# Kernel tuning notes

Hardware: AMD Instinct MI355X
Metric: run time of the kernel (lower is better)

## Reference

```python
import jax, jax.numpy as jnp
import numpy as np
from jax import lax

DIM = 1024
EXPAND = 2
D_STATE = 16
D_CONV = 4
DT_RANK = 64  # ceil(DIM/16)
DIM_INNER = DIM * EXPAND
B_SZ, SEQ = 2, 1024


def setup_inputs() -> dict:
    key = jax.random.key(0)
    ks = jax.random.split(key, 8)
    s = lambda fan_in: 1.0 / np.sqrt(fan_in)
    x = jax.random.normal(ks[0], (B_SZ, SEQ, DIM), dtype=jnp.float32)
    W_in = jax.random.normal(ks[1], (DIM, 2 * DIM_INNER), dtype=jnp.float32) * s(DIM)
    conv_w = jax.random.normal(ks[2], (DIM_INNER, D_CONV), dtype=jnp.float32) * s(D_CONV)
    conv_b = jax.random.normal(ks[3], (DIM_INNER,), dtype=jnp.float32) * s(D_CONV)
    W_x = jax.random.normal(ks[4], (DIM_INNER, DT_RANK + 2 * D_STATE), dtype=jnp.float32) * s(DIM_INNER)
    W_dt = jax.random.normal(ks[5], (DT_RANK, DIM_INNER), dtype=jnp.float32) * s(DT_RANK)
    b_dt = jax.random.normal(ks[6], (DIM_INNER,), dtype=jnp.float32) * s(DT_RANK)
    # A_log = log(repeat(arange(1, d_state+1), 'n -> d n'))
    A_log = jnp.broadcast_to(jnp.log(jnp.arange(1, D_STATE + 1, dtype=jnp.float32)), (DIM_INNER, D_STATE))
    D = jnp.ones((DIM_INNER,), dtype=jnp.float32)
    W_out = jax.random.normal(ks[7], (DIM_INNER, DIM), dtype=jnp.float32) * s(DIM_INNER)
    return {"x": x, "W_in": W_in, "conv_w": conv_w, "conv_b": conv_b,
            "W_x": W_x, "W_dt": W_dt, "b_dt": b_dt, "A_log": A_log, "D": D, "W_out": W_out}


def _mamba_forward(x, W_in, conv_w, conv_b, W_x, W_dt, b_dt, A_log, D, W_out):
    b, l, d = x.shape
    di = W_out.shape[0]  # dim_inner
    n = A_log.shape[1]   # d_state
    dt_rank = W_dt.shape[0]

    # in_proj (no bias) and split into ssm branch / gate residual
    x_and_res = x @ W_in                      # [b, l, 2*di]
    u, res = jnp.split(x_and_res, 2, axis=-1)  # each [b, l, di]

    # causal depthwise conv1d along sequence (torch pads both sides then slices [:l])
    pad = conv_w.shape[1] - 1
    up = jnp.pad(u, ((0, 0), (pad, 0), (0, 0)))
    kernel = conv_w.T[:, None, :]  # [W=d_conv, I=1, O=di]
    u = lax.conv_general_dilated(up, kernel, window_strides=(1,), padding='VALID',
                                 dimension_numbers=('NWC', 'WIO', 'NWC'),
                                 feature_group_count=di) + conv_b
    u = jax.nn.silu(u)  # [b, l, di]

    # input-dependent SSM params
    x_dbl = u @ W_x  # [b, l, dt_rank + 2n]
    delta_r, Bm, Cm = jnp.split(x_dbl, [dt_rank, dt_rank + n], axis=-1)
    delta = jax.nn.softplus(delta_r @ W_dt + b_dt)  # [b, l, di]
    A = -jnp.exp(A_log)  # [di, n]

    deltaA = jnp.exp(jnp.einsum('bld,dn->bldn', delta, A))        # [b, l, di, n]
    deltaB_u = jnp.einsum('bld,bln,bld->bldn', delta, Bm, u)       # [b, l, di, n]

    def step(h, inp):
        dA_t, dBu_t, c_t = inp            # [b,di,n], [b,di,n], [b,n]
        h = dA_t * h + dBu_t
        y_t = jnp.einsum('bdn,bn->bd', h, c_t)
        return h, y_t

    h0 = jnp.zeros((b, di, n), dtype=u.dtype)
    xs = (jnp.moveaxis(deltaA, 1, 0), jnp.moveaxis(deltaB_u, 1, 0), jnp.moveaxis(Cm, 1, 0))
    _, ys = lax.scan(step, h0, xs)        # ys: [l, b, di]
    y = jnp.moveaxis(ys, 0, 1)            # [b, l, di]
    y = y + u * D                          # skip term

    y = y * jax.nn.silu(res)               # gate
    return y @ W_out                       # [b, l, dim]


def reference(x, W_in, conv_w, conv_b, W_x, W_dt, b_dt, A_log, D, W_out):
    return _mamba_forward(x, W_in, conv_w, conv_b, W_x, W_dt, b_dt, A_log, D, W_out)
```

## Files before the change

kernel.cpp:

```cpp
#include <hip/hip_runtime.h>
#include <hip/hip_bf16.h>
#include <math.h>


__device__ __forceinline__ float silu_f(float x) {
    return x / (1.f + __expf(-x));
}
__device__ __forceinline__ unsigned short f2bf(float f) {
    __hip_bfloat16 h = __float2bfloat16(f);
    return *(unsigned short*)&h;
}
__device__ __forceinline__ float bf2f(unsigned short u) {
    return __uint_as_float((unsigned)u << 16);
}

typedef __attribute__((ext_vector_type(8))) short short8v;
typedef __attribute__((ext_vector_type(4))) float f32x4;

__device__ __forceinline__ void gload16(const void* g, void* lds) {
    __builtin_amdgcn_global_load_lds(
        (const __attribute__((address_space(1))) unsigned int*)g,
        (__attribute__((address_space(3))) unsigned int*)lds, 16, 0, 0);
}

template<int MODE>
__device__ __forceinline__ void gemm_core(
    const unsigned short* __restrict__ A,
    const unsigned short* __restrict__ BT,
    float* __restrict__ C, unsigned short* __restrict__ Cb,
    int M, int N, int K, int kbeg, int klen,
    int bx, int by, unsigned short* As, unsigned short* Bs)
{
    const int tid  = threadIdx.x;
    const int wid  = tid >> 6;
    const int lane = tid & 63;
    const int wr = wid >> 1, wc = wid & 1;
    const int row0 = by * 128, col0 = bx * 128;

    f32x4 acc[4][4] = {};

    const int srow = lane >> 2;
    const int scol = (lane & 3) * 8;

    for (int k0 = kbeg; k0 < kbeg + klen; k0 += 32) {
        #pragma unroll
        for (int c = 0; c < 2; ++c) {
            int chunk = wid * 2 + c;
            gload16(A  + (size_t)(row0 + chunk * 16 + srow) * K + k0 + scol,
                    (void*)(As + chunk * 512));
            gload16(BT + (size_t)(col0 + chunk * 16 + srow) * K + k0 + scol,
                    (void*)(Bs + chunk * 512));
        }
        __syncthreads();
        short8v a[4], b[4];
        #pragma unroll
        for (int i = 0; i < 4; ++i)
            a[i] = *(const short8v*)&As[(wr * 64 + i * 16 + (lane & 15)) * 32 + (lane >> 4) * 8];
        #pragma unroll
        for (int j = 0; j < 4; ++j)
            b[j] = *(const short8v*)&Bs[(wc * 64 + j * 16 + (lane & 15)) * 32 + (lane >> 4) * 8];
        #pragma unroll
        for (int i = 0; i < 4; ++i)
            #pragma unroll
            for (int j = 0; j < 4; ++j)
                acc[i][j] = __builtin_amdgcn_mfma_f32_16x16x32_bf16(a[i], b[j], acc[i][j], 0, 0, 0);
        __syncthreads();
    }

    #pragma unroll
    for (int i = 0; i < 4; ++i) {
        int rbase = row0 + wr * 64 + i * 16 + (lane >> 4) * 4;
        #pragma unroll
        for (int j = 0; j < 4; ++j) {
            int cc = col0 + wc * 64 + j * 16 + (lane & 15);
            #pragma unroll
            for (int r = 0; r < 4; ++r) {
                float v = acc[i][j][r];
                if (MODE == 0) {
                    C[(size_t)(rbase + r) * N + cc] = v;
                } else {
                    unsigned short m = f2bf(v);
                    unsigned other = (unsigned)__shfl_xor((int)m, 1, 64) & 0xffffu;
                    if (!(lane & 1))
                        *(unsigned*)(Cb + (size_t)(rbase + r) * N + cc) =
                            (unsigned)m | (other << 16);
                }
            }
        }
    }
}

__global__ __launch_bounds__(256) void gemm7_swz(
    const unsigned short* __restrict__ A,
    const unsigned short* __restrict__ BT,
    unsigned short* __restrict__ Pb)
{
    __shared__ unsigned short As[128 * 32];
    __shared__ unsigned short Bs[128 * 32];
    const int bid = blockIdx.x;
    const int xcd = bid & 7, idx = bid >> 3;
    const int kz = xcd >> 1;
    const int by = (xcd & 1) * 8 + (idx >> 3);
    const int bx = idx & 7;
    gemm_core<4>(A, BT, nullptr, Pb + (size_t)kz * 2048 * 1024,
                 2048, 1024, 2048, kz * 512, 512, bx, by, As, Bs);
}

template<int MODE>
__global__ __launch_bounds__(256) void gemm64_bf16(
    const unsigned short* __restrict__ A,
    const unsigned short* __restrict__ BT,
    unsigned short* __restrict__ Cb,
    const float* __restrict__ bias,
    int M, int N, int K, int klen)
{
    __shared__ unsigned short As[64 * 32];
    __shared__ unsigned short Bs[64 * 32];
    const int tid  = threadIdx.x;
    const int wid  = tid >> 6;
    const int lane = tid & 63;
    const int wr = wid >> 1, wc = wid & 1;
    const int row0 = blockIdx.y * 64, col0 = blockIdx.x * 64;
    const int kbeg = blockIdx.z * klen;
    if (MODE == 5) Cb += (size_t)blockIdx.z * M * N;

    f32x4 acc[2][2] = {};
    const int srow = lane >> 2;
    const int scol = (lane & 3) * 8;

    for (int k0 = kbeg; k0 < kbeg + klen; k0 += 32) {
        gload16(A  + (size_t)(row0 + wid * 16 + srow) * K + k0 + scol,
                (void*)(As + wid * 512));
        gload16(BT + (size_t)(col0 + wid * 16 + srow) * K + k0 + scol,
                (void*)(Bs + wid * 512));
        __syncthreads();
        short8v a[2], b[2];
        #pragma unroll
        for (int i = 0; i < 2; ++i)
            a[i] = *(const short8v*)&As[(wr * 32 + i * 16 + (lane & 15)) * 32 + (lane >> 4) * 8];
        #pragma unroll
        for (int j = 0; j < 2; ++j)
            b[j] = *(const short8v*)&Bs[(wc * 32 + j * 16 + (lane & 15)) * 32 + (lane >> 4) * 8];
        #pragma unroll
        for (int i = 0; i < 2; ++i)
            #pragma unroll
            for (int j = 0; j < 2; ++j)
                acc[i][j] = __builtin_amdgcn_mfma_f32_16x16x32_bf16(a[i], b[j], acc[i][j], 0, 0, 0);
        __syncthreads();
    }

    #pragma unroll
    for (int i = 0; i < 2; ++i) {
        int rbase = row0 + wr * 32 + i * 16 + (lane >> 4) * 4;
        #pragma unroll
        for (int j = 0; j < 2; ++j) {
            int cc = col0 + wc * 32 + j * 16 + (lane & 15);
            float bi = (MODE == 3) ? bias[cc] : 0.f;
            #pragma unroll
            for (int r = 0; r < 4; ++r) {
                float v = acc[i][j][r];
                if (MODE == 3) {
                    v += bi;
                    v = (v > 20.f) ? v : __logf(1.f + __expf(v));
                }
                unsigned short m = f2bf(v);
                unsigned other = (unsigned)__shfl_xor((int)m, 1, 64) & 0xffffu;
                if (!(lane & 1))
                    *(unsigned*)(Cb + (size_t)(rbase + r) * N + cc) =
                        (unsigned)m | (other << 16);
            }
        }
    }
}

__device__ __forceinline__ void trans64(
    const float* __restrict__ W, unsigned short* __restrict__ WT,
    int K, int N, int bk, int bn, int tid, float (*t)[65])
{
    const int tx = tid & 63, ty = tid >> 6;
    #pragma unroll
    for (int s = 0; s < 16; ++s)
        t[ty + 4 * s][tx] = W[(size_t)(bk + ty + 4 * s) * N + bn + tx];
    __syncthreads();
    const int c = tid & 31, rg = tid >> 5;
    #pragma unroll
    for (int s = 0; s < 8; ++s) {
        int r = rg + 8 * s;
        unsigned lo = f2bf(t[2 * c][r]);
        unsigned hi = f2bf(t[2 * c + 1][r]);
        *(unsigned*)(WT + (size_t)(bn + r) * K + bk + 2 * c) = lo | (hi << 16);
    }
}

__global__ __launch_bounds__(256) void gemm1_fused(
    const unsigned short* __restrict__ xb,
    const unsigned short* __restrict__ W_inT,
    unsigned short* __restrict__ xrb,
    const float* __restrict__ W_out,
    const float* __restrict__ Wx,
    const float* __restrict__ Wdt,
    unsigned short* __restrict__ W_outT,
    unsigned short* __restrict__ W_xTp,
    unsigned short* __restrict__ W_dtTp)
{
    __shared__ char smem[64 * 65 * 4];
    const int bid = blockIdx.x;
    const int tid = threadIdx.x;
    if (bid < 512) {
        unsigned short* As = (unsigned short*)smem;
        unsigned short* Bs = As + 128 * 32;
        const int xcd = bid & 7, idx = bid >> 3;
        const int bx = (xcd & 3) * 8 + (idx & 7);
        const int by = (xcd >> 2) * 8 + (idx >> 3);
        gemm_core<4>(xb, W_inT, nullptr, xrb,
                     2048, 4096, 1024, 0, 1024, bx, by, As, Bs);
    } else if (bid < 1024) {
        int tt = bid - 512;
        trans64(W_out, W_outT, 2048, 1024, (tt >> 4) * 64, (tt & 15) * 64,
                tid, (float(*)[65])smem);
    } else if (bid < 1280) {
        int idx4 = (bid - 1024) * 256 + tid;
        int n = idx4 >> 9, k0 = (idx4 & 511) << 2;
        ushort4 o;
        o.x = f2bf((n < 96) ? Wx[(size_t)(k0 + 0) * 96 + n] : 0.f);
        o.y = f2bf((n < 96) ? Wx[(size_t)(k0 + 1) * 96 + n] : 0.f);
        o.z = f2bf((n < 96) ? Wx[(size_t)(k0 + 2) * 96 + n] : 0.f);
        o.w = f2bf((n < 96) ? Wx[(size_t)(k0 + 3) * 96 + n] : 0.f);
        *(ushort4*)(W_xTp + (size_t)idx4 * 4) = o;
    } else {
        int idx4 = (bid - 1280) * 256 + tid;
        int n = idx4 >> 5, k0 = (idx4 & 31) << 2;
        ushort4 o;
        o.x = f2bf((k0 + 0 < 64) ? Wdt[(size_t)(k0 + 0) * 2048 + n] : 0.f);
        o.y = f2bf((k0 + 1 < 64) ? Wdt[(size_t)(k0 + 1) * 2048 + n] : 0.f);
        o.z = f2bf((k0 + 2 < 64) ? Wdt[(size_t)(k0 + 2) * 2048 + n] : 0.f);
        o.w = f2bf((k0 + 3 < 64) ? Wdt[(size_t)(k0 + 3) * 2048 + n] : 0.f);
        *(ushort4*)(W_dtTp + (size_t)idx4 * 4) = o;
    }
}

__global__ __launch_bounds__(256) void prep(
    const float* __restrict__ x,
    const float* __restrict__ W_in,
    unsigned short* __restrict__ xb,
    unsigned short* __restrict__ W_inT)
{
    __shared__ float t[64][65];
    const int bid = blockIdx.x;
    const int tid = threadIdx.x;
    if (bid < 1024) {
        int i = bid * 256 + tid;
        float4 v0 = *(const float4*)(x + (size_t)i * 8);
        float4 v1 = *(const float4*)(x + (size_t)i * 8 + 4);
        ushort4 o0, o1;
        o0.x = f2bf(v0.x); o0.y = f2bf(v0.y); o0.z = f2bf(v0.z); o0.w = f2bf(v0.w);
        o1.x = f2bf(v1.x); o1.y = f2bf(v1.y); o1.z = f2bf(v1.z); o1.w = f2bf(v1.w);
        *(ushort4*)(xb + (size_t)i * 8) = o0;
        *(ushort4*)(xb + (size_t)i * 8 + 4) = o1;
    } else {
        int tt = bid - 1024;
        trans64(W_in, W_inT, 1024, 4096, (tt >> 6) * 64, (tt & 63) * 64, tid, t);
    }
}

__global__ __launch_bounds__(256) void reduce16(
    const unsigned short* __restrict__ P, unsigned short* __restrict__ dstb)
{
    int i = blockIdx.x * 256 + threadIdx.x;
    float s[8] = {};
    #pragma unroll
    for (int k = 0; k < 16; ++k) {
        uint4 v = ((const uint4*)P)[i + (size_t)k * 32768];
        const unsigned short* pv = (const unsigned short*)&v;
        #pragma unroll
        for (int e = 0; e < 8; ++e) s[e] += bf2f(pv[e]);
    }
    unsigned short ob[8];
    #pragma unroll
    for (int e = 0; e < 8; ++e) ob[e] = f2bf(s[e]);
    ((uint4*)dstb)[i] = *(const uint4*)ob;
}

__global__ __launch_bounds__(256) void reduce4(
    const unsigned short* __restrict__ P, float* __restrict__ dst)
{
    int i = blockIdx.x * 256 + threadIdx.x;
    float s[8] = {};
    #pragma unroll
    for (int k = 0; k < 4; ++k) {
        uint4 v = ((const uint4*)P)[i + (size_t)k * 262144];
        const unsigned short* pv = (const unsigned short*)&v;
        #pragma unroll
        for (int e = 0; e < 8; ++e) s[e] += bf2f(pv[e]);
    }
    ((float4*)dst)[i * 2]     = make_float4(s[0], s[1], s[2], s[3]);
    ((float4*)dst)[i * 2 + 1] = make_float4(s[4], s[5], s[6], s[7]);
}

__global__ __launch_bounds__(256) void conv_silu(
    const unsigned short* __restrict__ xrb,
    const float* __restrict__ conv_w,
    const float* __restrict__ conv_b,
    unsigned short* __restrict__ ub)
{
    int t = blockIdx.x * 256 + threadIdx.x;
    int d4 = (t & 511) << 2;
    int r = t >> 9;
    int l = r & 1023, b = r >> 10;
    float4 cb4 = *(const float4*)(conv_b + d4);
    float acc[4] = {cb4.x, cb4.y, cb4.z, cb4.w};
    float4 cw0 = *(const float4*)(conv_w + (size_t)(d4 + 0) * 4);
    float4 cw1 = *(const float4*)(conv_w + (size_t)(d4 + 1) * 4);
    float4 cw2 = *(const float4*)(conv_w + (size_t)(d4 + 2) * 4);
    float4 cw3 = *(const float4*)(conv_w + (size_t)(d4 + 3) * 4);
    float w0a[4] = {cw0.x, cw0.y, cw0.z, cw0.w};
    float w1a[4] = {cw1.x, cw1.y, cw1.z, cw1.w};
    float w2a[4] = {cw2.x, cw2.y, cw2.z, cw2.w};
    float w3a[4] = {cw3.x, cw3.y, cw3.z, cw3.w};
    #pragma unroll
    for (int w = 0; w < 4; ++w) {
        int ls = l + w - 3;
        if (ls >= 0) {
            ushort4 xv = *(const ushort4*)(xrb + (((size_t)((b << 10) + ls)) << 12) + d4);
            acc[0] = fmaf(bf2f(xv.x), w0a[w], acc[0]);
            acc[1] = fmaf(bf2f(xv.y), w1a[w], acc[1]);
            acc[2] = fmaf(bf2f(xv.z), w2a[w], acc[2]);
            acc[3] = fmaf(bf2f(xv.w), w3a[w], acc[3]);
        }
    }
    ushort4 o;
    o.x = f2bf(silu_f(acc[0]));
    o.y = f2bf(silu_f(acc[1]));
    o.z = f2bf(silu_f(acc[2]));
    o.w = f2bf(silu_f(acc[3]));
    *(ushort4*)(ub + (size_t)t * 4) = o;
}

#define SCAN_T 16
#define NSEG 8
#define SEGLEN 128

#define DPP_ADD(v, ctrl) ((v) + __int_as_float(__builtin_amdgcn_update_dpp( \
        0, __float_as_int(v), (ctrl), 0xF, 0xF, true)))

__global__ __launch_bounds__(256) void scan_pass1(
    const unsigned short* __restrict__ delta_b,
    const unsigned short* __restrict__ ub,
    const unsigned short* __restrict__ xdbl_b,
    const float* __restrict__ A_log,
    float* __restrict__ stash)
{
    __shared__ float2 du[2][SCAN_T][17];
    __shared__ float  bs[2][SCAN_T][17];

    const int tid = threadIdx.x;
    const int dg = blockIdx.x, b = blockIdx.y, s = blockIdx.z;
    const int d0 = dg * 16;
    const int ch = tid >> 4, n = tid & 15;
    const float Aval = -__expf(A_log[(d0 + ch) * 16 + n]);
    const int sli = tid >> 4, sc = tid & 15;
    const int lbase = s * SEGLEN;

    float g_d, g_u, g_b;
    {
        size_t row = (size_t)(b << 10) + lbase + sli;
        g_d = bf2f(delta_b[(row << 11) + d0 + sc]);
        g_u = bf2f(ub[(row << 11) + d0 + sc]);
        g_b = bf2f(xdbl_b[(row << 7) + 64 + sc]);
    }
    du[0][sli][sc] = make_float2(g_d, g_u);
    bs[0][sli][sc] = g_b;
    __syncthreads();

    float h = 0.f, sd = 0.f;
    int cb = 0;
    for (int c = 0; c < SEGLEN / SCAN_T; ++c) {
        const bool more = (c + 1) < SEGLEN / SCAN_T;
        if (more) {
            size_t row = (size_t)(b << 10) + lbase + (c + 1) * SCAN_T + sli;
            g_d = bf2f(delta_b[(row << 11) + d0 + sc]);
            g_u = bf2f(ub[(row << 11) + d0 + sc]);
            g_b = bf2f(xdbl_b[(row << 7) + 64 + sc]);
        }
        float e_[SCAN_T], f_[SCAN_T];
        #pragma unroll
        for (int li = 0; li < SCAN_T; ++li) {
            float2 duv = du[cb][li][ch];
            float bv = bs[cb][li][n];
            e_[li] = __expf(duv.x * Aval);
            f_[li] = duv.x * bv * duv.y;
            sd += duv.x;
        }
        #pragma unroll
        for (int li = 0; li < SCAN_T; ++li)
            h = fmaf(e_[li], h, f_[li]);
        if (more) {
            du[cb ^ 1][sli][sc] = make_float2(g_d, g_u);
            bs[cb ^ 1][sli][sc] = g_b;
        }
        __syncthreads();
        cb ^= 1;
    }
    int j = (((b << 3) + s) * 128 + dg) * 256 + tid;
    stash[j] = __expf(Aval * sd);
    stash[j + 524288] = h;
}

__global__ __launch_bounds__(256) void scan_pass3(
    const unsigned short* __restrict__ delta_b,
    const unsigned short* __restrict__ ub,
    const unsigned short* __restrict__ xdbl_b,
    const float* __restrict__ A_log,
    const unsigned short* __restrict__ xrb,
    const float* __restrict__ stash,
    const float* __restrict__ Dv,
    unsigned short* __restrict__ ysb)
{
    __shared__ float2 du[2][SCAN_T][17];
    __shared__ float2 bc[2][SCAN_T][17];
    __shared__ float  rs[2][SCAN_T][17];

    const int tid = threadIdx.x;
    const int dg = blockIdx.x, b = blockIdx.y, s = blockIdx.z;
    const int d0 = dg * 16;
    const int ch = tid >> 4, n = tid & 15;
    const float Aval = -__expf(A_log[(d0 + ch) * 16 + n]);
    const float Dval = Dv[d0 + ch];
    const int sli = tid >> 4, sc = tid & 15;
    const int lbase = s * SEGLEN;

    float h = 0.f;
    for (int sp = 0; sp < s; ++sp) {
        int j = (((b << 3) + sp) * 128 + dg) * 256 + tid;
        h = fmaf(stash[j], h, stash[j + 524288]);
    }

    float g_d, g_u, g_b, g_c, g_r;
    {
        size_t row = (size_t)(b << 10) + lbase + sli;
        g_d = bf2f(delta_b[(row << 11) + d0 + sc]);
        g_u = bf2f(ub[(row << 11) + d0 + sc]);
        g_b = bf2f(xdbl_b[(row << 7) + 64 + sc]);
        g_c = bf2f(xdbl_b[(row << 7) + 80 + sc]);
        g_r = bf2f(xrb[(row << 12) + 2048 + d0 + sc]);
    }
    du[0][sli][sc] = make_float2(g_d, g_u);
    bc[0][sli][sc] = make_float2(g_b, g_c);
    rs[0][sli][sc] = g_r;
    __syncthreads();

    int cb = 0;
    for (int c = 0; c < SEGLEN / SCAN_T; ++c) {
        const int l0 = lbase + c * SCAN_T;
        const bool more = (c + 1) < SEGLEN / SCAN_T;
        if (more) {
            size_t row = (size_t)(b << 10) + l0 + SCAN_T + sli;
            g_d = bf2f(delta_b[(row << 11) + d0 + sc]);
            g_u = bf2f(ub[(row << 11) + d0 + sc]);
            g_b = bf2f(xdbl_b[(row << 7) + 64 + sc]);
            g_c = bf2f(xdbl_b[(row << 7) + 80 + sc]);
            g_r = bf2f(xrb[(row << 12) + 2048 + d0 + sc]);
        }
        float e_[SCAN_T], f_[SCAN_T], c_[SCAN_T];
        #pragma unroll
        for (int li = 0; li < SCAN_T; ++li) {
            float2 duv = du[cb][li][ch];
            float2 bcv = bc[cb][li][n];
            e_[li] = __expf(duv.x * Aval);
            f_[li] = duv.x * bcv.x * duv.y;
            c_[li] = bcv.y;
        }
        float mysum = 0.f;
        #pragma unroll
        for (int li = 0; li < SCAN_T; ++li) {
            h = fmaf(e_[li], h, f_[li]);
            float pv = h * c_[li];
            pv = DPP_ADD(pv, 0xB1);
            pv = DPP_ADD(pv, 0x4E);
            pv = DPP_ADD(pv, 0x141);
            pv = DPP_ADD(pv, 0x140);
            mysum = (n == li) ? pv : mysum;
        }
        {
            float2 duv = du[cb][n][ch];
            float resv = rs[cb][n][ch];
            float outv = (mysum + duv.y * Dval) * silu_f(resv);
            ysb[((size_t)((b << 10) + l0 + n) << 11) + d0 + ch] = f2bf(outv);
        }
        if (more) {
            du[cb ^ 1][sli][sc] = make_float2(g_d, g_u);
            bc[cb ^ 1][sli][sc] = make_float2(g_b, g_c);
            rs[cb ^ 1][sli][sc] = g_r;
        }
        __syncthreads();
        cb ^= 1;
    }
}

extern "C" void kernel_launch(void* const* d_in, const int* in_sizes, int n_in,
                              void* d_out, int out_size, void* d_ws, size_t ws_size,
                              hipStream_t stream)
{
    const float* x      = (const float*)d_in[0];
    const float* W_in   = (const float*)d_in[1];
    const float* conv_w = (const float*)d_in[2];
    const float* conv_b = (const float*)d_in[3];
    const float* W_x    = (const float*)d_in[4];
    const float* W_dt   = (const float*)d_in[5];
    const float* b_dt   = (const float*)d_in[6];
    const float* A_log  = (const float*)d_in[7];
    const float* Dv     = (const float*)d_in[8];
    const float* W_out  = (const float*)d_in[9];
    float* out = (float*)d_out;

    float* ws    = (float*)d_ws;
    unsigned short* P16b = (unsigned short*)(ws + (size_t)262144);
    unsigned short* P4b  = (unsigned short*)(ws + (size_t)4456448);
    float* stash = ws + (size_t)12845056;
    unsigned short* bfr = (unsigned short*)(ws + (size_t)13893632);
    unsigned short* xb      = bfr;
    unsigned short* W_inT   = bfr + (size_t)2097152;
    unsigned short* W_xTp   = bfr + (size_t)6291456;
    unsigned short* W_dtTp  = bfr + (size_t)6553600;
    unsigned short* W_outT  = bfr + (size_t)6815744;
    unsigned short* xrb     = bfr + (size_t)8912896;
    unsigned short* ub      = bfr + (size_t)17301504;
    unsigned short* delta_b = bfr + (size_t)21495808;
    unsigned short* ysb     = bfr + (size_t)25690112;
    unsigned short* xdbl_b  = bfr + (size_t)29884416;

    prep<<<2048, 256, 0, stream>>>(x, W_in, xb, W_inT);
    gemm1_fused<<<1536, 256, 0, stream>>>(xb, W_inT, xrb, W_out, W_x, W_dt,
                                          W_outT, W_xTp, W_dtTp);
    conv_silu<<<4096, 256, 0, stream>>>(xrb, conv_w, conv_b, ub);
    gemm64_bf16<5><<<dim3(2, 32, 16), 256, 0, stream>>>(ub, W_xTp, P16b, nullptr, 2048, 128, 2048, 128);
    reduce16<<<128, 256, 0, stream>>>(P16b, xdbl_b);
    gemm64_bf16<3><<<dim3(32, 32, 1), 256, 0, stream>>>(xdbl_b, W_dtTp, delta_b, b_dt, 2048, 2048, 128, 128);
    scan_pass1<<<dim3(128, 2, 8), 256, 0, stream>>>(delta_b, ub, xdbl_b, A_log, stash);
    scan_pass3<<<dim3(128, 2, 8), 256, 0, stream>>>(delta_b, ub, xdbl_b, A_log, xrb, stash, Dv, ysb);
    gemm7_swz<<<512, 256, 0, stream>>>(ysb, W_outT, P4b);
    reduce4<<<1024, 256, 0, stream>>>(P4b, out);
}
```

Baseline: 144.2 us.

## Split-K the input projection GEMM into two partial outputs summed by consumers

The in_proj GEMM now runs as two K-halves across twice as many blocks, each writing its own bf16 partial buffer. The conv_silu and scan_pass3 consumers read both partials and add them, so no separate reduce kernel is needed. This is meant to raise occupancy and parallelism for the first GEMM on the many-CU device. In exchange, the xr intermediate carries twice the memory traffic, and rounding each partial to bf16 before the sum adds some error.

```diff
diff --git a/kernel.cpp b/kernel.cpp
--- a/kernel.cpp
+++ b/kernel.cpp
@@ -195,7 +195,7 @@
 __global__ __launch_bounds__(256) void gemm1_fused(
     const unsigned short* __restrict__ xb,
     const unsigned short* __restrict__ W_inT,
-    unsigned short* __restrict__ xrb,
+    unsigned short* __restrict__ xr_p,
     const float* __restrict__ W_out,
     const float* __restrict__ Wx,
     const float* __restrict__ Wdt,
@@ -206,20 +206,22 @@
     __shared__ char smem[64 * 65 * 4];
     const int bid = blockIdx.x;
     const int tid = threadIdx.x;
-    if (bid < 512) {
+    if (bid < 1024) {
         unsigned short* As = (unsigned short*)smem;
         unsigned short* Bs = As + 128 * 32;
         const int xcd = bid & 7, idx = bid >> 3;
-        const int bx = (xcd & 3) * 8 + (idx & 7);
-        const int by = (xcd >> 2) * 8 + (idx >> 3);
-        gemm_core<4>(xb, W_inT, nullptr, xrb,
-                     2048, 4096, 1024, 0, 1024, bx, by, As, Bs);
-    } else if (bid < 1024) {
-        int tt = bid - 512;
+        const int kz = idx >> 6;
+        const int i  = idx & 63;
+        const int bx = (xcd & 3) * 8 + (i & 7);
+        const int by = (xcd >> 2) * 8 + (i >> 3);
+        gemm_core<4>(xb, W_inT, nullptr, xr_p + (size_t)kz * 2048 * 4096,
+                     2048, 4096, 1024, kz * 512, 512, bx, by, As, Bs);
+    } else if (bid < 1536) {
+        int tt = bid - 1024;
         trans64(W_out, W_outT, 2048, 1024, (tt >> 4) * 64, (tt & 15) * 64,
                 tid, (float(*)[65])smem);
-    } else if (bid < 1280) {
-        int idx4 = (bid - 1024) * 256 + tid;
+    } else if (bid < 1792) {
+        int idx4 = (bid - 1536) * 256 + tid;
         int n = idx4 >> 9, k0 = (idx4 & 511) << 2;
         ushort4 o;
         o.x = f2bf((n < 96) ? Wx[(size_t)(k0 + 0) * 96 + n] : 0.f);
@@ -228,7 +230,7 @@
         o.w = f2bf((n < 96) ? Wx[(size_t)(k0 + 3) * 96 + n] : 0.f);
         *(ushort4*)(W_xTp + (size_t)idx4 * 4) = o;
     } else {
-        int idx4 = (bid - 1280) * 256 + tid;
+        int idx4 = (bid - 1792) * 256 + tid;
         int n = idx4 >> 5, k0 = (idx4 & 31) << 2;
         ushort4 o;
         o.x = f2bf((k0 + 0 < 64) ? Wdt[(size_t)(k0 + 0) * 2048 + n] : 0.f);
@@ -298,7 +300,8 @@
 }
 
 __global__ __launch_bounds__(256) void conv_silu(
-    const unsigned short* __restrict__ xrb,
+    const unsigned short* __restrict__ xp0,
+    const unsigned short* __restrict__ xp1,
     const float* __restrict__ conv_w,
     const float* __restrict__ conv_b,
     unsigned short* __restrict__ ub)
@@ -321,11 +324,13 @@
     for (int w = 0; w < 4; ++w) {
         int ls = l + w - 3;
         if (ls >= 0) {
-            ushort4 xv = *(const ushort4*)(xrb + (((size_t)((b << 10) + ls)) << 12) + d4);
-            acc[0] = fmaf(bf2f(xv.x), w0a[w], acc[0]);
-            acc[1] = fmaf(bf2f(xv.y), w1a[w], acc[1]);
-            acc[2] = fmaf(bf2f(xv.z), w2a[w], acc[2]);
-            acc[3] = fmaf(bf2f(xv.w), w3a[w], acc[3]);
+            size_t off = (((size_t)((b << 10) + ls)) << 12) + d4;
+            ushort4 x0 = *(const ushort4*)(xp0 + off);
+            ushort4 x1 = *(const ushort4*)(xp1 + off);
+            acc[0] = fmaf(bf2f(x0.x) + bf2f(x1.x), w0a[w], acc[0]);
+            acc[1] = fmaf(bf2f(x0.y) + bf2f(x1.y), w1a[w], acc[1]);
+            acc[2] = fmaf(bf2f(x0.z) + bf2f(x1.z), w2a[w], acc[2]);
+            acc[3] = fmaf(bf2f(x0.w) + bf2f(x1.w), w3a[w], acc[3]);
         }
     }
     ushort4 o;
@@ -411,7 +416,8 @@
     const unsigned short* __restrict__ ub,
     const unsigned short* __restrict__ xdbl_b,
     const float* __restrict__ A_log,
-    const unsigned short* __restrict__ xrb,
+    const unsigned short* __restrict__ xp0,
+    const unsigned short* __restrict__ xp1,
     const float* __restrict__ stash,
     const float* __restrict__ Dv,
     unsigned short* __restrict__ ysb)
@@ -442,7 +448,8 @@
         g_u = bf2f(ub[(row << 11) + d0 + sc]);
         g_b = bf2f(xdbl_b[(row << 7) + 64 + sc]);
         g_c = bf2f(xdbl_b[(row << 7) + 80 + sc]);
-        g_r = bf2f(xrb[(row << 12) + 2048 + d0 + sc]);
+        size_t roff = (row << 12) + 2048 + d0 + sc;
+        g_r = bf2f(xp0[roff]) + bf2f(xp1[roff]);
     }
     du[0][sli][sc] = make_float2(g_d, g_u);
     bc[0][sli][sc] = make_float2(g_b, g_c);
@@ -459,7 +466,8 @@
             g_u = bf2f(ub[(row << 11) + d0 + sc]);
             g_b = bf2f(xdbl_b[(row << 7) + 64 + sc]);
             g_c = bf2f(xdbl_b[(row << 7) + 80 + sc]);
-            g_r = bf2f(xrb[(row << 12) + 2048 + d0 + sc]);
+            size_t roff = (row << 12) + 2048 + d0 + sc;
+            g_r = bf2f(xp0[roff]) + bf2f(xp1[roff]);
         }
         float e_[SCAN_T], f_[SCAN_T], c_[SCAN_T];
         #pragma unroll
@@ -523,21 +531,23 @@
     unsigned short* W_xTp   = bfr + (size_t)6291456;
     unsigned short* W_dtTp  = bfr + (size_t)6553600;
     unsigned short* W_outT  = bfr + (size_t)6815744;
-    unsigned short* xrb     = bfr + (size_t)8912896;
-    unsigned short* ub      = bfr + (size_t)17301504;
-    unsigned short* delta_b = bfr + (size_t)21495808;
-    unsigned short* ysb     = bfr + (size_t)25690112;
-    unsigned short* xdbl_b  = bfr + (size_t)29884416;
+    unsigned short* xr_p    = bfr + (size_t)8912896;
+    unsigned short* xp0     = xr_p;
+    unsigned short* xp1     = xr_p + (size_t)8388608;
+    unsigned short* ub      = bfr + (size_t)25690112;
+    unsigned short* delta_b = bfr + (size_t)29884416;
+    unsigned short* ysb     = bfr + (size_t)34078720;
+    unsigned short* xdbl_b  = bfr + (size_t)38273024;
 
     prep<<<2048, 256, 0, stream>>>(x, W_in, xb, W_inT);
-    gemm1_fused<<<1536, 256, 0, stream>>>(xb, W_inT, xrb, W_out, W_x, W_dt,
+    gemm1_fused<<<2048, 256, 0, stream>>>(xb, W_inT, xr_p, W_out, W_x, W_dt,
                                           W_outT, W_xTp, W_dtTp);
-    conv_silu<<<4096, 256, 0, stream>>>(xrb, conv_w, conv_b, ub);
+    conv_silu<<<4096, 256, 0, stream>>>(xp0, xp1, conv_w, conv_b, ub);
     gemm64_bf16<5><<<dim3(2, 32, 16), 256, 0, stream>>>(ub, W_xTp, P16b, nullptr, 2048, 128, 2048, 128);
     reduce16<<<128, 256, 0, stream>>>(P16b, xdbl_b);
     gemm64_bf16<3><<<dim3(32, 32, 1), 256, 0, stream>>>(xdbl_b, W_dtTp, delta_b, b_dt, 2048, 2048, 128, 128);
     scan_pass1<<<dim3(128, 2, 8), 256, 0, stream>>>(delta_b, ub, xdbl_b, A_log, stash);
-    scan_pass3<<<dim3(128, 2, 8), 256, 0, stream>>>(delta_b, ub, xdbl_b, A_log, xrb, stash, Dv, ysb);
+    scan_pass3<<<dim3(128, 2, 8), 256, 0, stream>>>(delta_b, ub, xdbl_b, A_log, xp0, xp1, stash, Dv, ysb);
     gemm7_swz<<<512, 256, 0, stream>>>(ysb, W_outT, P4b);
     reduce4<<<1024, 256, 0, stream>>>(P4b, out);
 }
```

New measurement: 154.6 us. +7.2%, slower.

## Triple-buffer LDS tiles in shared GEMM core with async prefetch

Applied to the files above, without the earlier changes.

The bf16 MFMA GEMM core now keeps three LDS stages of A/B tiles. It prefetches tiles three k-steps ahead with global_load_lds, using explicit vmcnt waits and raw barriers in place of two __syncthreads per iteration. The goal is to hide global-load latency behind MFMA work. This triples LDS use per block to 48KB, which may lower occupancy, and it relies on hand-counted outstanding loads being correct.

```diff
diff --git a/kernel.cpp b/kernel.cpp
--- a/kernel.cpp
+++ b/kernel.cpp
@@ -41,30 +41,55 @@
 
     const int srow = lane >> 2;
     const int scol = (lane & 3) * 8;
-
-    for (int k0 = kbeg; k0 < kbeg + klen; k0 += 32) {
+    const int T = klen >> 5;
+
+    #pragma unroll
+    for (int t = 0; t < 3; ++t) {
         #pragma unroll
         for (int c = 0; c < 2; ++c) {
             int chunk = wid * 2 + c;
-            gload16(A  + (size_t)(row0 + chunk * 16 + srow) * K + k0 + scol,
-                    (void*)(As + chunk * 512));
-            gload16(BT + (size_t)(col0 + chunk * 16 + srow) * K + k0 + scol,
-                    (void*)(Bs + chunk * 512));
-        }
-        __syncthreads();
+            gload16(A  + (size_t)(row0 + chunk * 16 + srow) * K + (kbeg + t * 32) + scol,
+                    (void*)(As + t * 4096 + chunk * 512));
+            gload16(BT + (size_t)(col0 + chunk * 16 + srow) * K + (kbeg + t * 32) + scol,
+                    (void*)(Bs + t * 4096 + chunk * 512));
+        }
+    }
+    asm volatile("s_waitcnt vmcnt(8)" ::: "memory");
+    __builtin_amdgcn_s_barrier();
+
+    for (int i = 0; i < T; ++i) {
+        const int cur = i % 3;
         short8v a[4], b[4];
         #pragma unroll
-        for (int i = 0; i < 4; ++i)
-            a[i] = *(const short8v*)&As[(wr * 64 + i * 16 + (lane & 15)) * 32 + (lane >> 4) * 8];
+        for (int ii = 0; ii < 4; ++ii)
+            a[ii] = *(const short8v*)&As[cur * 4096 + (wr * 64 + ii * 16 + (lane & 15)) * 32 + (lane >> 4) * 8];
         #pragma unroll
         for (int j = 0; j < 4; ++j)
-            b[j] = *(const short8v*)&Bs[(wc * 64 + j * 16 + (lane & 15)) * 32 + (lane >> 4) * 8];
-        #pragma unroll
-        for (int i = 0; i < 4; ++i)
+            b[j] = *(const short8v*)&Bs[cur * 4096 + (wc * 64 + j * 16 + (lane & 15)) * 32 + (lane >> 4) * 8];
+        asm volatile("s_waitcnt lgkmcnt(0)" ::: "memory");
+        __builtin_amdgcn_s_barrier();
+        if (i + 3 < T) {
+            #pragma unroll
+            for (int c = 0; c < 2; ++c) {
+                int chunk = wid * 2 + c;
+                gload16(A  + (size_t)(row0 + chunk * 16 + srow) * K + (kbeg + (i + 3) * 32) + scol,
+                        (void*)(As + cur * 4096 + chunk * 512));
+                gload16(BT + (size_t)(col0 + chunk * 16 + srow) * K + (kbeg + (i + 3) * 32) + scol,
+                        (void*)(Bs + cur * 4096 + chunk * 512));
+            }
+        }
+        #pragma unroll
+        for (int ii = 0; ii < 4; ++ii)
             #pragma unroll
             for (int j = 0; j < 4; ++j)
-                acc[i][j] = __builtin_amdgcn_mfma_f32_16x16x32_bf16(a[i], b[j], acc[i][j], 0, 0, 0);
-        __syncthreads();
+                acc[ii][j] = __builtin_amdgcn_mfma_f32_16x16x32_bf16(a[ii], b[j], acc[ii][j], 0, 0, 0);
+        if (i < T - 3)
+            asm volatile("s_waitcnt vmcnt(8)" ::: "memory");
+        else if (i == T - 3)
+            asm volatile("s_waitcnt vmcnt(4)" ::: "memory");
+        else
+            asm volatile("s_waitcnt vmcnt(0)" ::: "memory");
+        __builtin_amdgcn_s_barrier();
     }
 
     #pragma unroll
@@ -95,8 +120,8 @@
     const unsigned short* __restrict__ BT,
     unsigned short* __restrict__ Pb)
 {
-    __shared__ unsigned short As[128 * 32];
-    __shared__ unsigned short Bs[128 * 32];
+    __shared__ unsigned short As[3 * 4096];
+    __shared__ unsigned short Bs[3 * 4096];
     const int bid = blockIdx.x;
     const int xcd = bid & 7, idx = bid >> 3;
     const int kz = xcd >> 1;
@@ -203,12 +228,12 @@
     unsigned short* __restrict__ W_xTp,
     unsigned short* __restrict__ W_dtTp)
 {
-    __shared__ char smem[64 * 65 * 4];
+    __shared__ char smem[49152];
     const int bid = blockIdx.x;
     const int tid = threadIdx.x;
     if (bid < 512) {
         unsigned short* As = (unsigned short*)smem;
-        unsigned short* Bs = As + 128 * 32;
+        unsigned short* Bs = As + 12288;
         const int xcd = bid & 7, idx = bid >> 3;
         const int bx = (xcd & 3) * 8 + (idx & 7);
         const int by = (xcd >> 2) * 8 + (idx >> 3);
```

Result: no change. 144.7 us (+0.3%).
